# Performance work log

Measured on AMD Instinct MI355X. Metric: run time of the kernel, lower is better.

Reference implementation:

```python
import jax, jax.numpy as jnp
import numpy as np

N_NODES = 50000   # n_nodes (adjacency is [N,N])
NNZ = 800000      # nonzeros per support (avg degree 16)
S = 3             # number of supports
D_IN = 512
D_OUT = 256


def setup_inputs() -> dict:
    key = jax.random.key(0)
    k0, k1, k2, k3, k4, k5 = jax.random.split(key, 6)
    x = jax.random.normal(k0, (N_NODES, D_IN), dtype=jnp.float32)
    # glorot-uniform per-support weights, stacked [S, D_IN, D_OUT]
    scale = float(np.sqrt(6.0 / (D_IN + D_OUT)))
    W = jax.random.uniform(k1, (S, D_IN, D_OUT), dtype=jnp.float32, minval=-scale, maxval=scale)
    rows = jax.random.randint(k2, (S, NNZ), 0, N_NODES, dtype=jnp.int32)
    cols = jax.random.randint(k3, (S, NNZ), 0, N_NODES, dtype=jnp.int32)
    vals = jax.random.uniform(k4, (S, NNZ), dtype=jnp.float32)
    # Conv1d(in=S, out=1, k=1, bias=False) == learned weighted sum over supports
    cw = jax.random.normal(k5, (S,), dtype=jnp.float32) * 0.5
    return {"x": x, "W": W, "rows": rows, "cols": cols, "vals": vals, "cw": cw}


def reference(x, W, rows, cols, vals, cw):
    # mod='output': out = relu( sum_i cw[i] * (A_i @ (x @ W_i)) )
    def spmm(r, c, v, pre):
        # A in COO: out[r] += v * pre[c]
        msgs = v[:, None] * pre[c]          # [NNZ, D_OUT] gather
        return jax.ops.segment_sum(msgs, r, num_segments=N_NODES)

    out = jnp.zeros((N_NODES, D_OUT), dtype=x.dtype)
    for i in range(S):                      # small fixed support count
        pre = x @ W[i]                      # dense GEMM [N, D_OUT]
        out = out + cw[i] * spmm(rows[i], cols[i], vals[i], pre)
    return jax.nn.relu(out)
```

## Files before the change

kernel.cpp:

```cpp
#include <hip/hip_runtime.h>
#include <stdint.h>

#define N_NODES 50000
#define N_PAD   50048
#define NNZ     800000
#define SUP     3
#define D_IN    512
#define D_OUT   256
#define TOT_E   (SUP * NNZ)
#define NBUCK   391
#define CAP     6976
#define CHUNK   6144

typedef __attribute__((ext_vector_type(8))) short bf16x8;
typedef __attribute__((ext_vector_type(4))) float f32x4;
typedef __attribute__((address_space(3))) unsigned int lds_u32_t;
typedef const __attribute__((address_space(1))) unsigned int glb_u32_t;

static __device__ __forceinline__ unsigned short f2bf(float f) {
    unsigned int u = __float_as_uint(f);
    unsigned int r = (u + 0x7fffu + ((u >> 16) & 1u)) >> 16;
    return (unsigned short)r;
}
static __device__ __forceinline__ unsigned int pack_bf2(float lo, float hi) {
    unsigned int a = __float_as_uint(lo) + 0x8000u;
    unsigned int b = __float_as_uint(hi) + 0x8000u;
    return (a >> 16) | (b & 0xffff0000u);
}
static __device__ __forceinline__ float bf2f(unsigned short h) {
    return __uint_as_float(((unsigned int)h) << 16);
}

__global__ void xprep_kernel(const float* __restrict__ x, unsigned int* __restrict__ xb) {
    int idx = blockIdx.x * 256 + threadIdx.x;
    if (idx >= N_NODES * D_IN / 8) return;
    const float4* src = (const float4*)(x) + idx * 2;
    float4 f0 = src[0];
    float4 f1 = src[1];
    uint4 o;
    o.x = pack_bf2(f0.x, f0.y);
    o.y = pack_bf2(f0.z, f0.w);
    o.z = pack_bf2(f1.x, f1.y);
    o.w = pack_bf2(f1.z, f1.w);
    *((uint4*)xb + idx) = o;
}

__global__ void wprep_kernel(const float* __restrict__ W, unsigned short* __restrict__ Wt) {
    int idx = blockIdx.x * 256 + threadIdx.x;
    if (idx >= SUP * D_IN * D_OUT) return;
    int n = idx & (D_OUT - 1);
    int k = (idx >> 8) & (D_IN - 1);
    int s = idx >> 17;
    Wt[((size_t)s * D_OUT + n) * D_IN + k] = f2bf(W[idx]);
}

__global__ __launch_bounds__(256) void bucket_kernel(const int* __restrict__ rows,
                                                     const int* __restrict__ cols,
                                                     const float* __restrict__ vals,
                                                     const float* __restrict__ cw,
                                                     int* __restrict__ bucket_cursor,
                                                     int2* __restrict__ buck) {
    __shared__ int hist[NBUCK];
    __shared__ int sc[256];
    __shared__ int sstart[NBUCK];
    __shared__ int lcur[NBUCK];
    __shared__ int gbase[NBUCK];
    __shared__ unsigned short bucket_of[CHUNK];
    __shared__ int2 stage[CHUNK];

    const int tid = threadIdx.x;
    const int base_n = blockIdx.x * CHUNK;
    const int count = min(CHUNK, TOT_E - base_n);
    float cw0 = cw[0], cw1 = cw[1], cw2 = cw[2];

    for (int i = tid; i < NBUCK; i += 256) hist[i] = 0;
    __syncthreads();
    for (int i = tid; i < count; i += 256) {
        atomicAdd(&hist[rows[base_n + i] >> 7], 1);
    }
    __syncthreads();
    int b0 = 2 * tid, b1 = b0 + 1;
    int h0 = (b0 < NBUCK) ? hist[b0] : 0;
    int h1 = (b1 < NBUCK) ? hist[b1] : 0;
    sc[tid] = h0 + h1;
    __syncthreads();
    for (int off = 1; off < 256; off <<= 1) {
        int t = (tid >= off) ? sc[tid - off] : 0;
        __syncthreads();
        sc[tid] += t;
        __syncthreads();
    }
    int excl = sc[tid] - (h0 + h1);
    if (b0 < NBUCK) { sstart[b0] = excl;      lcur[b0] = excl; }
    if (b1 < NBUCK) { sstart[b1] = excl + h0; lcur[b1] = excl + h0; }
    for (int i = tid; i < NBUCK; i += 256)
        gbase[i] = atomicAdd(&bucket_cursor[i], hist[i]);
    __syncthreads();
    for (int i = tid; i < count; i += 256) {
        int n = base_n + i;
        int r = rows[n];
        int c = cols[n];
        float v = vals[n];
        int s = n / NNZ;
        float w = v * (s == 0 ? cw0 : (s == 1 ? cw1 : cw2));
        int b = r >> 7;
        int p = atomicAdd(&lcur[b], 1);
        stage[p] = make_int2(((r & 127) << 18) | (s * N_NODES + c), __float_as_int(w));
        bucket_of[p] = (unsigned short)b;
    }
    __syncthreads();
    for (int i = tid; i < count; i += 256) {
        int b = bucket_of[i];
        int local_off = i - sstart[b];
        buck[(size_t)b * CAP + gbase[b] + local_off] = stage[i];
    }
}

__global__ __launch_bounds__(256) void sort_kernel(const int2* __restrict__ buck,
                                                   const int* __restrict__ bucket_cursor,
                                                   int2* __restrict__ cv,
                                                   int* __restrict__ base,
                                                   int* __restrict__ cnt) {
    __shared__ int hist[128];
    __shared__ int sc[128];
    __shared__ int sstart[128];
    __shared__ int cur[128];
    __shared__ int2 stage[CAP];

    const int b = blockIdx.x;
    const int tid = threadIdx.x;
    const int sz = bucket_cursor[b];
    const int2* src = buck + (size_t)b * CAP;

    if (tid < 128) hist[tid] = 0;
    __syncthreads();
    for (int i = tid; i < sz; i += 256) {
        atomicAdd(&hist[((unsigned)src[i].x) >> 18], 1);
    }
    __syncthreads();
    if (tid < 128) sc[tid] = hist[tid];
    __syncthreads();
    for (int off = 1; off < 128; off <<= 1) {
        int t = (tid >= off && tid < 128) ? sc[tid - off] : 0;
        __syncthreads();
        if (tid < 128) sc[tid] += t;
        __syncthreads();
    }
    if (tid < 128) {
        int st = sc[tid] - hist[tid];
        sstart[tid] = st;
        cur[tid] = st;
    }
    __syncthreads();
    for (int i = tid; i < sz; i += 256) {
        int2 e = src[i];
        int rl = ((unsigned)e.x) >> 18;
        int p = atomicAdd(&cur[rl], 1);
        stage[p] = make_int2(e.x & 0x3FFFF, e.y);
    }
    __syncthreads();
    size_t gb = (size_t)b * CAP;
    for (int i = tid; i < sz; i += 256) cv[gb + i] = stage[i];
    int r = b * 128 + tid;
    if (tid < 128 && r < N_NODES) {
        base[r] = (int)gb + sstart[tid];
        cnt[r]  = hist[tid];
    }
}

__global__ __launch_bounds__(256) void gemm_kernel(const unsigned short* __restrict__ xb,
                                                   const unsigned short* __restrict__ Wt,
                                                   unsigned short* __restrict__ pre) {
    __shared__ unsigned short lds_a[128 * 64];
    __shared__ unsigned short lds_b[128 * 64];
    const int m0 = blockIdx.y * 128;
    const int n0 = (blockIdx.x & 1) * 128;
    const int s  = blockIdx.x >> 1;
    const unsigned short* wt = Wt + (size_t)s * D_OUT * D_IN;
    const int tid  = threadIdx.x;
    const int wave = tid >> 6;
    const int lane = tid & 63;
    const int quad = lane >> 4;
    const int lo   = lane & 15;
    const int wm = (wave & 1) * 64;
    const int wn = (wave >> 1) * 64;

    f32x4 acc[4][4] = {};

    for (int kb = 0; kb < D_IN; kb += 64) {
        __syncthreads();
        #pragma unroll
        for (int c = 0; c < 4; ++c) {
            int idx = c * 256 + tid;
            int row = idx >> 3;
            int kp  = idx & 7;
            const unsigned short* ga = xb + (size_t)(m0 + row) * D_IN + kb + kp * 8;
            __builtin_amdgcn_global_load_lds((glb_u32_t*)ga,
                                             (lds_u32_t*)&lds_a[idx * 8], 16, 0, 0);
            const unsigned short* gb = wt + (size_t)(n0 + row) * D_IN + kb + kp * 8;
            __builtin_amdgcn_global_load_lds((glb_u32_t*)gb,
                                             (lds_u32_t*)&lds_b[idx * 8], 16, 0, 0);
        }
        __syncthreads();

        #pragma unroll
        for (int t = 0; t < 2; ++t) {
            bf16x8 af[4], bfr[4];
            #pragma unroll
            for (int i = 0; i < 4; ++i)
                af[i] = *(const bf16x8*)&lds_a[(wm + 16 * i + lo) * 64 + t * 32 + quad * 8];
            #pragma unroll
            for (int j = 0; j < 4; ++j)
                bfr[j] = *(const bf16x8*)&lds_b[(wn + 16 * j + lo) * 64 + t * 32 + quad * 8];
            #pragma unroll
            for (int i = 0; i < 4; ++i)
                #pragma unroll
                for (int j = 0; j < 4; ++j)
                    acc[i][j] = __builtin_amdgcn_mfma_f32_16x16x32_bf16(af[i], bfr[j], acc[i][j], 0, 0, 0);
        }
    }

    #pragma unroll
    for (int i = 0; i < 4; ++i) {
        #pragma unroll
        for (int j = 0; j < 4; ++j) {
            int gn = n0 + wn + 16 * j + lo;
            #pragma unroll
            for (int r = 0; r < 4; ++r) {
                int gm2 = m0 + wm + 16 * i + quad * 4 + r;
                if (gm2 < N_NODES)
                    pre[((size_t)s * N_NODES + gm2) * D_OUT + gn] = f2bf(acc[i][j][r]);
            }
        }
    }
}

__global__ __launch_bounds__(256) void spmm_kernel(const unsigned short* __restrict__ pre,
                                                   const int* __restrict__ base,
                                                   const int* __restrict__ cnt,
                                                   const int2* __restrict__ cv,
                                                   float* __restrict__ out) {
    int row  = blockIdx.x * 4 + (threadIdx.x >> 6);
    int lane = threadIdx.x & 63;
    int start = base[row];
    int end   = start + cnt[row];
    float a0 = 0.f, a1 = 0.f, a2 = 0.f, a3 = 0.f;
    int j = start;
    for (; j + 8 <= end; j += 8) {
        int2 e[8];
        #pragma unroll
        for (int q = 0; q < 8; ++q) e[q] = cv[j + q];
        ushort4 p[8];
        #pragma unroll
        for (int q = 0; q < 8; ++q)
            p[q] = *(const ushort4*)(pre + (size_t)e[q].x * D_OUT + lane * 4);
        #pragma unroll
        for (int q = 0; q < 8; ++q) {
            float w = __int_as_float(e[q].y);
            a0 += w * bf2f(p[q].x);
            a1 += w * bf2f(p[q].y);
            a2 += w * bf2f(p[q].z);
            a3 += w * bf2f(p[q].w);
        }
    }
    for (; j + 4 <= end; j += 4) {
        int2 e[4];
        #pragma unroll
        for (int q = 0; q < 4; ++q) e[q] = cv[j + q];
        ushort4 p[4];
        #pragma unroll
        for (int q = 0; q < 4; ++q)
            p[q] = *(const ushort4*)(pre + (size_t)e[q].x * D_OUT + lane * 4);
        #pragma unroll
        for (int q = 0; q < 4; ++q) {
            float w = __int_as_float(e[q].y);
            a0 += w * bf2f(p[q].x);
            a1 += w * bf2f(p[q].y);
            a2 += w * bf2f(p[q].z);
            a3 += w * bf2f(p[q].w);
        }
    }
    for (; j < end; ++j) {
        int2 e = cv[j];
        float w = __int_as_float(e.y);
        ushort4 p = *(const ushort4*)(pre + (size_t)e.x * D_OUT + lane * 4);
        a0 += w * bf2f(p.x);
        a1 += w * bf2f(p.y);
        a2 += w * bf2f(p.z);
        a3 += w * bf2f(p.w);
    }
    float4 o = make_float4(fmaxf(a0, 0.f), fmaxf(a1, 0.f), fmaxf(a2, 0.f), fmaxf(a3, 0.f));
    *(float4*)(out + (size_t)row * D_OUT + lane * 4) = o;
}

extern "C" void kernel_launch(void* const* d_in, const int* in_sizes, int n_in,
                              void* d_out, int out_size, void* d_ws, size_t ws_size,
                              hipStream_t stream) {
    const float* x    = (const float*)d_in[0];
    const float* W    = (const float*)d_in[1];
    const int*   rows = (const int*)d_in[2];
    const int*   cols = (const int*)d_in[3];
    const float* vals = (const float*)d_in[4];
    const float* cw   = (const float*)d_in[5];
    float* out = (float*)d_out;

    char* ws = (char*)d_ws;
    size_t off = 0;
    auto alloc = [&](size_t bytes) -> void* {
        void* p = ws + off;
        off += (bytes + 255) & ~(size_t)255;
        return p;
    };
    unsigned short* pre  = (unsigned short*)alloc((size_t)SUP * N_NODES * D_OUT * 2);
    unsigned short* xb   = (unsigned short*)alloc((size_t)N_PAD * D_IN * 2);
    unsigned short* Wt   = (unsigned short*)alloc((size_t)SUP * D_OUT * D_IN * 2);
    int* base            = (int*)alloc((size_t)N_NODES * 4);
    int* cnt             = (int*)alloc((size_t)N_NODES * 4);
    int* bucket_cursor   = (int*)alloc((size_t)NBUCK * 4);
    int2* cv             = (int2*)alloc((size_t)NBUCK * CAP * 8);
    int2* buck           = (int2*)pre;

    hipMemsetAsync(bucket_cursor, 0, (size_t)NBUCK * 4, stream);

    bucket_kernel<<<(TOT_E + CHUNK - 1) / CHUNK, 256, 0, stream>>>(rows, cols, vals, cw,
                                                                   bucket_cursor, buck);
    sort_kernel<<<NBUCK, 256, 0, stream>>>(buck, bucket_cursor, cv, base, cnt);
    xprep_kernel<<<(N_NODES * D_IN / 8 + 255) / 256, 256, 0, stream>>>(x, (unsigned int*)xb);
    wprep_kernel<<<(SUP * D_IN * D_OUT + 255) / 256, 256, 0, stream>>>(W, Wt);
    gemm_kernel<<<dim3(6, 391), 256, 0, stream>>>(xb, Wt, pre);
    spmm_kernel<<<N_NODES / 4, 256, 0, stream>>>(pre, base, cnt, cv, out);
}
```

Before: 493.0 us.

## Fuse prep and sort/GEMM kernels into block-partitioned launches to overlap work

Merges bucketing, weight conversion and x conversion into one kernel partitioned by block index, and merges the per-bucket sort with the dense GEMM into a second kernel. This removes launch gaps and lets independent stages run concurrently on the GPU. The bucket staging buffer moves from the pre buffer to the output buffer so the GEMM can write pre while sorting reads buckets. The trade-off is that every block reserves the largest shared-memory footprint, which may lower occupancy for the light conversion blocks and the GEMM blocks.

```diff
diff --git a/kernel.cpp b/kernel.cpp
--- a/kernel.cpp
+++ b/kernel.cpp
@@ -11,6 +11,9 @@
 #define NBUCK   391
 #define CAP     6976
 #define CHUNK   6144
+#define NB_WPREP 1536
+#define NB_XPREP 12500
+#define NB_GEMM  2346
 
 typedef __attribute__((ext_vector_type(8))) short bf16x8;
 typedef __attribute__((ext_vector_type(4))) float f32x4;
@@ -31,205 +34,214 @@
     return __uint_as_float(((unsigned int)h) << 16);
 }
 
-__global__ void xprep_kernel(const float* __restrict__ x, unsigned int* __restrict__ xb) {
-    int idx = blockIdx.x * 256 + threadIdx.x;
-    if (idx >= N_NODES * D_IN / 8) return;
-    const float4* src = (const float4*)(x) + idx * 2;
-    float4 f0 = src[0];
-    float4 f1 = src[1];
-    uint4 o;
-    o.x = pack_bf2(f0.x, f0.y);
-    o.y = pack_bf2(f0.z, f0.w);
-    o.z = pack_bf2(f1.x, f1.y);
-    o.w = pack_bf2(f1.z, f1.w);
-    *((uint4*)xb + idx) = o;
-}
-
-__global__ void wprep_kernel(const float* __restrict__ W, unsigned short* __restrict__ Wt) {
-    int idx = blockIdx.x * 256 + threadIdx.x;
-    if (idx >= SUP * D_IN * D_OUT) return;
-    int n = idx & (D_OUT - 1);
-    int k = (idx >> 8) & (D_IN - 1);
-    int s = idx >> 17;
-    Wt[((size_t)s * D_OUT + n) * D_IN + k] = f2bf(W[idx]);
-}
-
-__global__ __launch_bounds__(256) void bucket_kernel(const int* __restrict__ rows,
-                                                     const int* __restrict__ cols,
-                                                     const float* __restrict__ vals,
-                                                     const float* __restrict__ cw,
-                                                     int* __restrict__ bucket_cursor,
-                                                     int2* __restrict__ buck) {
-    __shared__ int hist[NBUCK];
-    __shared__ int sc[256];
-    __shared__ int sstart[NBUCK];
-    __shared__ int lcur[NBUCK];
-    __shared__ int gbase[NBUCK];
-    __shared__ unsigned short bucket_of[CHUNK];
-    __shared__ int2 stage[CHUNK];
-
+__global__ __launch_bounds__(256) void prep_kernel(const int* __restrict__ rows,
+                                                   const int* __restrict__ cols,
+                                                   const float* __restrict__ vals,
+                                                   const float* __restrict__ cw,
+                                                   int* __restrict__ bucket_cursor,
+                                                   int2* __restrict__ buck,
+                                                   const float* __restrict__ x,
+                                                   unsigned int* __restrict__ xb,
+                                                   const float* __restrict__ W,
+                                                   unsigned short* __restrict__ Wt) {
+    __shared__ double smem8[8590];
+    char* smem = (char*)smem8;
+    const int blk = blockIdx.x;
     const int tid = threadIdx.x;
-    const int base_n = blockIdx.x * CHUNK;
-    const int count = min(CHUNK, TOT_E - base_n);
-    float cw0 = cw[0], cw1 = cw[1], cw2 = cw[2];
-
-    for (int i = tid; i < NBUCK; i += 256) hist[i] = 0;
-    __syncthreads();
-    for (int i = tid; i < count; i += 256) {
-        atomicAdd(&hist[rows[base_n + i] >> 7], 1);
-    }
-    __syncthreads();
-    int b0 = 2 * tid, b1 = b0 + 1;
-    int h0 = (b0 < NBUCK) ? hist[b0] : 0;
-    int h1 = (b1 < NBUCK) ? hist[b1] : 0;
-    sc[tid] = h0 + h1;
-    __syncthreads();
-    for (int off = 1; off < 256; off <<= 1) {
-        int t = (tid >= off) ? sc[tid - off] : 0;
-        __syncthreads();
-        sc[tid] += t;
-        __syncthreads();
-    }
-    int excl = sc[tid] - (h0 + h1);
-    if (b0 < NBUCK) { sstart[b0] = excl;      lcur[b0] = excl; }
-    if (b1 < NBUCK) { sstart[b1] = excl + h0; lcur[b1] = excl + h0; }
-    for (int i = tid; i < NBUCK; i += 256)
-        gbase[i] = atomicAdd(&bucket_cursor[i], hist[i]);
-    __syncthreads();
-    for (int i = tid; i < count; i += 256) {
-        int n = base_n + i;
-        int r = rows[n];
-        int c = cols[n];
-        float v = vals[n];
-        int s = n / NNZ;
-        float w = v * (s == 0 ? cw0 : (s == 1 ? cw1 : cw2));
-        int b = r >> 7;
-        int p = atomicAdd(&lcur[b], 1);
-        stage[p] = make_int2(((r & 127) << 18) | (s * N_NODES + c), __float_as_int(w));
-        bucket_of[p] = (unsigned short)b;
-    }
-    __syncthreads();
-    for (int i = tid; i < count; i += 256) {
-        int b = bucket_of[i];
-        int local_off = i - sstart[b];
-        buck[(size_t)b * CAP + gbase[b] + local_off] = stage[i];
-    }
-}
-
-__global__ __launch_bounds__(256) void sort_kernel(const int2* __restrict__ buck,
-                                                   const int* __restrict__ bucket_cursor,
-                                                   int2* __restrict__ cv,
-                                                   int* __restrict__ base,
-                                                   int* __restrict__ cnt) {
-    __shared__ int hist[128];
-    __shared__ int sc[128];
-    __shared__ int sstart[128];
-    __shared__ int cur[128];
-    __shared__ int2 stage[CAP];
-
-    const int b = blockIdx.x;
+
+    if (blk < NBUCK) {
+        int2* stage = (int2*)smem;
+        unsigned short* bucket_of = (unsigned short*)(smem + 49152);
+        int* hist   = (int*)(smem + 61440);
+        int* sc     = hist + NBUCK;
+        int* sstart = sc + 256;
+        int* lcur   = sstart + NBUCK;
+        int* gbase  = lcur + NBUCK;
+
+        const int base_n = blk * CHUNK;
+        const int count = min(CHUNK, TOT_E - base_n);
+        float cw0 = cw[0], cw1 = cw[1], cw2 = cw[2];
+
+        for (int i = tid; i < NBUCK; i += 256) hist[i] = 0;
+        __syncthreads();
+        for (int i = tid; i < count; i += 256)
+            atomicAdd(&hist[rows[base_n + i] >> 7], 1);
+        __syncthreads();
+        int b0 = 2 * tid, b1 = b0 + 1;
+        int h0 = (b0 < NBUCK) ? hist[b0] : 0;
+        int h1 = (b1 < NBUCK) ? hist[b1] : 0;
+        sc[tid] = h0 + h1;
+        __syncthreads();
+        for (int off = 1; off < 256; off <<= 1) {
+            int t = (tid >= off) ? sc[tid - off] : 0;
+            __syncthreads();
+            sc[tid] += t;
+            __syncthreads();
+        }
+        int excl = sc[tid] - (h0 + h1);
+        if (b0 < NBUCK) { sstart[b0] = excl;      lcur[b0] = excl; }
+        if (b1 < NBUCK) { sstart[b1] = excl + h0; lcur[b1] = excl + h0; }
+        for (int i = tid; i < NBUCK; i += 256)
+            gbase[i] = atomicAdd(&bucket_cursor[i], hist[i]);
+        __syncthreads();
+        for (int i = tid; i < count; i += 256) {
+            int n = base_n + i;
+            int r = rows[n];
+            int c = cols[n];
+            float v = vals[n];
+            int s = n / NNZ;
+            float w = v * (s == 0 ? cw0 : (s == 1 ? cw1 : cw2));
+            int b = r >> 7;
+            int p = atomicAdd(&lcur[b], 1);
+            stage[p] = make_int2(((r & 127) << 18) | (s * N_NODES + c), __float_as_int(w));
+            bucket_of[p] = (unsigned short)b;
+        }
+        __syncthreads();
+        for (int i = tid; i < count; i += 256) {
+            int b = bucket_of[i];
+            int local_off = i - sstart[b];
+            buck[(size_t)b * CAP + gbase[b] + local_off] = stage[i];
+        }
+    } else if (blk < NBUCK + NB_WPREP) {
+        int idx = (blk - NBUCK) * 256 + tid;
+        int n = idx & (D_OUT - 1);
+        int k = (idx >> 8) & (D_IN - 1);
+        int s = idx >> 17;
+        Wt[((size_t)s * D_OUT + n) * D_IN + k] = f2bf(W[idx]);
+    } else {
+        int idx = (blk - NBUCK - NB_WPREP) * 256 + tid;
+        const float4* src = (const float4*)(x) + idx * 2;
+        float4 f0 = src[0];
+        float4 f1 = src[1];
+        uint4 o;
+        o.x = pack_bf2(f0.x, f0.y);
+        o.y = pack_bf2(f0.z, f0.w);
+        o.z = pack_bf2(f1.x, f1.y);
+        o.w = pack_bf2(f1.z, f1.w);
+        *((uint4*)xb + idx) = o;
+    }
+}
+
+__global__ __launch_bounds__(256) void sortgemm_kernel(const int2* __restrict__ buck,
+                                                       const int* __restrict__ bucket_cursor,
+                                                       int2* __restrict__ cv,
+                                                       int* __restrict__ base,
+                                                       int* __restrict__ cnt,
+                                                       const unsigned short* __restrict__ xb,
+                                                       const unsigned short* __restrict__ Wt,
+                                                       unsigned short* __restrict__ pre) {
+    __shared__ double smem8[7232];
+    char* smem = (char*)smem8;
+    const int blk = blockIdx.x;
     const int tid = threadIdx.x;
-    const int sz = bucket_cursor[b];
-    const int2* src = buck + (size_t)b * CAP;
-
-    if (tid < 128) hist[tid] = 0;
-    __syncthreads();
-    for (int i = tid; i < sz; i += 256) {
-        atomicAdd(&hist[((unsigned)src[i].x) >> 18], 1);
-    }
-    __syncthreads();
-    if (tid < 128) sc[tid] = hist[tid];
-    __syncthreads();
-    for (int off = 1; off < 128; off <<= 1) {
-        int t = (tid >= off && tid < 128) ? sc[tid - off] : 0;
-        __syncthreads();
-        if (tid < 128) sc[tid] += t;
-        __syncthreads();
-    }
-    if (tid < 128) {
-        int st = sc[tid] - hist[tid];
-        sstart[tid] = st;
-        cur[tid] = st;
-    }
-    __syncthreads();
-    for (int i = tid; i < sz; i += 256) {
-        int2 e = src[i];
-        int rl = ((unsigned)e.x) >> 18;
-        int p = atomicAdd(&cur[rl], 1);
-        stage[p] = make_int2(e.x & 0x3FFFF, e.y);
-    }
-    __syncthreads();
-    size_t gb = (size_t)b * CAP;
-    for (int i = tid; i < sz; i += 256) cv[gb + i] = stage[i];
-    int r = b * 128 + tid;
-    if (tid < 128 && r < N_NODES) {
-        base[r] = (int)gb + sstart[tid];
-        cnt[r]  = hist[tid];
-    }
-}
-
-__global__ __launch_bounds__(256) void gemm_kernel(const unsigned short* __restrict__ xb,
-                                                   const unsigned short* __restrict__ Wt,
-                                                   unsigned short* __restrict__ pre) {
-    __shared__ unsigned short lds_a[128 * 64];
-    __shared__ unsigned short lds_b[128 * 64];
-    const int m0 = blockIdx.y * 128;
-    const int n0 = (blockIdx.x & 1) * 128;
-    const int s  = blockIdx.x >> 1;
-    const unsigned short* wt = Wt + (size_t)s * D_OUT * D_IN;
-    const int tid  = threadIdx.x;
-    const int wave = tid >> 6;
-    const int lane = tid & 63;
-    const int quad = lane >> 4;
-    const int lo   = lane & 15;
-    const int wm = (wave & 1) * 64;
-    const int wn = (wave >> 1) * 64;
-
-    f32x4 acc[4][4] = {};
-
-    for (int kb = 0; kb < D_IN; kb += 64) {
-        __syncthreads();
-        #pragma unroll
-        for (int c = 0; c < 4; ++c) {
-            int idx = c * 256 + tid;
-            int row = idx >> 3;
-            int kp  = idx & 7;
-            const unsigned short* ga = xb + (size_t)(m0 + row) * D_IN + kb + kp * 8;
-            __builtin_amdgcn_global_load_lds((glb_u32_t*)ga,
-                                             (lds_u32_t*)&lds_a[idx * 8], 16, 0, 0);
-            const unsigned short* gb = wt + (size_t)(n0 + row) * D_IN + kb + kp * 8;
-            __builtin_amdgcn_global_load_lds((glb_u32_t*)gb,
-                                             (lds_u32_t*)&lds_b[idx * 8], 16, 0, 0);
-        }
-        __syncthreads();
-
-        #pragma unroll
-        for (int t = 0; t < 2; ++t) {
-            bf16x8 af[4], bfr[4];
+
+    if (blk < NBUCK) {
+        int2* stage = (int2*)smem;
+        int* hist   = (int*)(smem + 55808);
+        int* sc     = hist + 128;
+        int* sstart = sc + 128;
+        int* cur    = sstart + 128;
+
+        const int b = blk;
+        const int sz = bucket_cursor[b];
+        const int2* src = buck + (size_t)b * CAP;
+
+        if (tid < 128) hist[tid] = 0;
+        __syncthreads();
+        for (int i = tid; i < sz; i += 256)
+            atomicAdd(&hist[((unsigned)src[i].x) >> 18], 1);
+        __syncthreads();
+        if (tid < 128) sc[tid] = hist[tid];
+        __syncthreads();
+        for (int off = 1; off < 128; off <<= 1) {
+            int t = (tid >= off && tid < 128) ? sc[tid - off] : 0;
+            __syncthreads();
+            if (tid < 128) sc[tid] += t;
+            __syncthreads();
+        }
+        if (tid < 128) {
+            int st = sc[tid] - hist[tid];
+            sstart[tid] = st;
+            cur[tid] = st;
+        }
+        __syncthreads();
+        for (int i = tid; i < sz; i += 256) {
+            int2 e = src[i];
+            int rl = ((unsigned)e.x) >> 18;
+            int p = atomicAdd(&cur[rl], 1);
+            stage[p] = make_int2(e.x & 0x3FFFF, e.y);
+        }
+        __syncthreads();
+        size_t gb = (size_t)b * CAP;
+        for (int i = tid; i < sz; i += 256) cv[gb + i] = stage[i];
+        int r = b * 128 + tid;
+        if (tid < 128 && r < N_NODES) {
+            base[r] = (int)gb + sstart[tid];
+            cnt[r]  = hist[tid];
+        }
+    } else {
+        unsigned short* lds_a = (unsigned short*)smem;
+        unsigned short* lds_b = (unsigned short*)(smem + 16384);
+        const int my  = blk - NBUCK;
+        const int mt  = my / 6;
+        const int rem = my % 6;
+        const int m0 = mt * 128;
+        const int n0 = (rem & 1) * 128;
+        const int s  = rem >> 1;
+        const unsigned short* wt = Wt + (size_t)s * D_OUT * D_IN;
+        const int wave = tid >> 6;
+        const int lane = tid & 63;
+        const int quad = lane >> 4;
+        const int lo   = lane & 15;
+        const int wm = (wave & 1) * 64;
+        const int wn = (wave >> 1) * 64;
+
+        f32x4 acc[4][4] = {};
+
+        for (int kb = 0; kb < D_IN; kb += 64) {
+            __syncthreads();
             #pragma unroll
-            for (int i = 0; i < 4; ++i)
-                af[i] = *(const bf16x8*)&lds_a[(wm + 16 * i + lo) * 64 + t * 32 + quad * 8];
+            for (int c = 0; c < 4; ++c) {
+                int idx = c * 256 + tid;
+                int row = idx >> 3;
+                int kp  = idx & 7;
+                const unsigned short* ga = xb + (size_t)(m0 + row) * D_IN + kb + kp * 8;
+                __builtin_amdgcn_global_load_lds((glb_u32_t*)ga,
+                                                 (lds_u32_t*)&lds_a[idx * 8], 16, 0, 0);
+                const unsigned short* gb = wt + (size_t)(n0 + row) * D_IN + kb + kp * 8;
+                __builtin_amdgcn_global_load_lds((glb_u32_t*)gb,
+                                                 (lds_u32_t*)&lds_b[idx * 8], 16, 0, 0);
+            }
+            __syncthreads();
+
             #pragma unroll
-            for (int j = 0; j < 4; ++j)
-                bfr[j] = *(const bf16x8*)&lds_b[(wn + 16 * j + lo) * 64 + t * 32 + quad * 8];
-            #pragma unroll
-            for (int i = 0; i < 4; ++i)
+            for (int t = 0; t < 2; ++t) {
+                bf16x8 af[4], bfr[4];
+                #pragma unroll
+                for (int i = 0; i < 4; ++i)
+                    af[i] = *(const bf16x8*)&lds_a[(wm + 16 * i + lo) * 64 + t * 32 + quad * 8];
                 #pragma unroll
                 for (int j = 0; j < 4; ++j)
-                    acc[i][j] = __builtin_amdgcn_mfma_f32_16x16x32_bf16(af[i], bfr[j], acc[i][j], 0, 0, 0);
-        }
-    }
-
-    #pragma unroll
-    for (int i = 0; i < 4; ++i) {
-        #pragma unroll
-        for (int j = 0; j < 4; ++j) {
-            int gn = n0 + wn + 16 * j + lo;
+                    bfr[j] = *(const bf16x8*)&lds_b[(wn + 16 * j + lo) * 64 + t * 32 + quad * 8];
+                #pragma unroll
+                for (int i = 0; i < 4; ++i)
+                    #pragma unroll
+                    for (int j = 0; j < 4; ++j)
+                        acc[i][j] = __builtin_amdgcn_mfma_f32_16x16x32_bf16(af[i], bfr[j], acc[i][j], 0, 0, 0);
+            }
+        }
+
+        #pragma unroll
+        for (int i = 0; i < 4; ++i) {
             #pragma unroll
-            for (int r = 0; r < 4; ++r) {
-                int gm2 = m0 + wm + 16 * i + quad * 4 + r;
-                if (gm2 < N_NODES)
-                    pre[((size_t)s * N_NODES + gm2) * D_OUT + gn] = f2bf(acc[i][j][r]);
+            for (int j = 0; j < 4; ++j) {
+                int gn = n0 + wn + 16 * j + lo;
+                #pragma unroll
+                for (int r = 0; r < 4; ++r) {
+                    int gm2 = m0 + wm + 16 * i + quad * 4 + r;
+                    if (gm2 < N_NODES)
+                        pre[((size_t)s * N_NODES + gm2) * D_OUT + gn] = f2bf(acc[i][j][r]);
+                }
             }
         }
     }
@@ -318,15 +330,13 @@
     int* cnt             = (int*)alloc((size_t)N_NODES * 4);
     int* bucket_cursor   = (int*)alloc((size_t)NBUCK * 4);
     int2* cv             = (int2*)alloc((size_t)NBUCK * CAP * 8);
-    int2* buck           = (int2*)pre;
+    int2* buck           = (int2*)d_out;
 
     hipMemsetAsync(bucket_cursor, 0, (size_t)NBUCK * 4, stream);
 
-    bucket_kernel<<<(TOT_E + CHUNK - 1) / CHUNK, 256, 0, stream>>>(rows, cols, vals, cw,
-                                                                   bucket_cursor, buck);
-    sort_kernel<<<NBUCK, 256, 0, stream>>>(buck, bucket_cursor, cv, base, cnt);
-    xprep_kernel<<<(N_NODES * D_IN / 8 + 255) / 256, 256, 0, stream>>>(x, (unsigned int*)xb);
-    wprep_kernel<<<(SUP * D_IN * D_OUT + 255) / 256, 256, 0, stream>>>(W, Wt);
-    gemm_kernel<<<dim3(6, 391), 256, 0, stream>>>(xb, Wt, pre);
+    prep_kernel<<<NBUCK + NB_WPREP + NB_XPREP, 256, 0, stream>>>(
+        rows, cols, vals, cw, bucket_cursor, buck, x, (unsigned int*)xb, W, Wt);
+    sortgemm_kernel<<<NBUCK + NB_GEMM, 256, 0, stream>>>(
+        buck, bucket_cursor, cv, base, cnt, xb, Wt, pre);
     spmm_kernel<<<N_NODES / 4, 256, 0, stream>>>(pre, base, cnt, cv, out);
 }
```

Result: faster. 474.5 us (-3.8%).
